# Kernel tuning notes

Measured on AMD Instinct MI355X. Metric: run time of the kernel, lower is better.

The kernel has to match this reference:

```python
import jax, jax.numpy as jnp
import numpy as np
from jax import lax

A = 15          # anchors per point
H = 34
W = 34
STRIDE = 8
ANCHOR_W = jnp.array([9.232984, 16.0, 27.712813, 18.465969, 32.0, 55.425626, 36.931937, 64.0, 110.851252, 73.863875, 128.0, 221.702503, 147.72775, 256.0, 443.405007], jnp.float32)
ANCHOR_H = jnp.array([27.72668, 16.0, 9.237604, 55.453359, 32.0, 18.475209, 110.906719, 64.0, 36.950417, 221.813438, 128.0, 73.900834, 443.626876, 256.0, 147.801669], jnp.float32)
BBOX_MEAN = jnp.array([0.000437, 0.002586, -0.123953, -0.081469], jnp.float32)
BBOX_STD = jnp.array([0.12677, 0.095741, 0.3173, 0.281042], jnp.float32)
THRESH = 0.2
MIN_H = 6.16056
MIN_W = 6.16056
MAX_CAND = 3000
TOP_N = 300
IOU_TH = 0.7
NEG = jnp.float32(-1e30)


def setup_inputs() -> dict:
    key = jax.random.key(0)
    k1, k2 = jax.random.split(key)
    return {
        "rpn_cls_prob_reshape": jax.random.uniform(k1, (1, 2 * A, H, W), jnp.float32),
        "rpn_bbox_pred": jax.random.normal(k2, (1, 4 * A, H, W), jnp.float32),
        "im_info": jnp.array([270, 270], jnp.int32),
    }


def reference(rpn_cls_prob_reshape, rpn_bbox_pred, im_info):
    origin_h = im_info[0].astype(jnp.float32)
    origin_w = im_info[1].astype(jnp.float32)
    # --- anchors: base boxes centered at origin, shifted over the grid ---
    xm = -0.5 * (ANCHOR_W - 1.0)
    ym = -0.5 * (ANCHOR_H - 1.0)
    base = jnp.stack([xm, ym, -xm, -ym], axis=1)  # [A,4] (xmin,ymin,xmax,ymax)
    sx = (jnp.arange(W) * STRIDE).astype(jnp.float32)
    sy = (jnp.arange(H) * STRIDE).astype(jnp.float32)
    SX, SY = jnp.meshgrid(sx, sy, indexing='ij')  # [W,H], matches torch meshgrid ij
    # original vstacks (shift_y, shift_x, shift_y, shift_x) -- replicate exactly
    shifts = jnp.stack([SY.ravel(), SX.ravel(), SY.ravel(), SX.ravel()], axis=1)  # [W*H,4]
    anchors = (shifts[:, None, :] + base[None, :, :]).reshape(-1, 4)  # [W*H*A,4]
    # --- bbox deltas: [1,4A,H,W] -> [(H*W*A),4] ---
    deltas = rpn_bbox_pred.reshape(A, 4, H, W).transpose(2, 3, 0, 1).reshape(-1, 4)
    deltas = deltas * BBOX_STD + BBOX_MEAN
    widths = anchors[:, 2] - anchors[:, 0] + 1.0
    heights = anchors[:, 3] - anchors[:, 1] + 1.0
    ctr_x = anchors[:, 0] + 0.5 * (widths - 1.0)
    ctr_y = anchors[:, 1] + 0.5 * (heights - 1.0)
    pcx = deltas[:, 0] * widths + ctr_x
    pcy = deltas[:, 1] * heights + ctr_y
    pw = jnp.exp(deltas[:, 2]) * widths
    ph = jnp.exp(deltas[:, 3]) * heights
    boxes = jnp.stack([pcx - 0.5 * (pw - 1.0), pcy - 0.5 * (ph - 1.0),
                       pcx + 0.5 * (pw - 1.0), pcy + 0.5 * (ph - 1.0)], axis=1)
    # --- clip to image (refine_out_of_map_bbox=True) ---
    boxes = jnp.stack([jnp.clip(boxes[:, 0], 0.0, origin_w - 1.0),
                       jnp.clip(boxes[:, 1], 0.0, origin_h - 1.0),
                       jnp.clip(boxes[:, 2], 0.0, origin_w - 1.0),
                       jnp.clip(boxes[:, 3], 0.0, origin_h - 1.0)], axis=1)
    # --- scores: [1,2A,H,W] -> [(H*W*A),2] ---
    scores = rpn_cls_prob_reshape.reshape(2, A, H * W).transpose(2, 1, 0).reshape(-1, 2)
    # --- filter: objectness threshold + HEIGHT_OR_WIDTH min size ---
    ws = boxes[:, 2] - boxes[:, 0] + 1.0
    hs = boxes[:, 3] - boxes[:, 1] + 1.0
    keep = (scores[:, 1] > THRESH) & ((ws >= MIN_W) | (hs >= MIN_H))
    masked = jnp.where(keep, scores[:, 1], NEG)
    top_vals, top_idx = lax.top_k(masked, MAX_CAND)
    cand_boxes = boxes[top_idx]       # [3000,4], sorted by desc score
    cand_scores = scores[top_idx]     # [3000,2]
    valid = top_vals > NEG * 0.5
    # --- greedy hard NMS (torchvision IoU convention, no +1) ---
    x1, y1, x2, y2 = cand_boxes[:, 0], cand_boxes[:, 1], cand_boxes[:, 2], cand_boxes[:, 3]
    areas = (x2 - x1) * (y2 - y1)
    iw = jnp.maximum(jnp.minimum(x2[:, None], x2[None, :]) - jnp.maximum(x1[:, None], x1[None, :]), 0.0)
    ih = jnp.maximum(jnp.minimum(y2[:, None], y2[None, :]) - jnp.maximum(y1[:, None], y1[None, :]), 0.0)
    inter = iw * ih
    iou = lax.stop_gradient(inter / jnp.maximum(areas[:, None] + areas[None, :] - inter, jnp.float32(1e-12)))
    pos = jnp.arange(MAX_CAND)

    def body(i, kp):
        sup = kp[i] & (iou[i] > IOU_TH) & (pos > i)
        return kp & ~sup

    kp = lax.fori_loop(0, MAX_CAND, body, valid)
    # --- take first top_n kept (score order preserved); pad with zeros ---
    sel = jnp.nonzero(kp, size=TOP_N, fill_value=MAX_CAND)[0]
    boxes_p = jnp.concatenate([cand_boxes, jnp.zeros((1, 4), cand_boxes.dtype)], axis=0)
    scores_p = jnp.concatenate([cand_scores, jnp.zeros((1, 2), cand_scores.dtype)], axis=0)
    out_boxes = boxes_p[sel]
    out_scores = scores_p[sel]
    proposals = jnp.concatenate([jnp.zeros((TOP_N, 1), out_boxes.dtype), out_boxes], axis=1)  # [300,5]
    return proposals, out_scores
```

## Files before the change

kernel.cpp:

```cpp
#include <hip/hip_runtime.h>
#include <stdint.h>

#define A 15
#define H_ 34
#define W_ 34
#define HW (H_*W_)
#define N (A*HW)
#define MAX_CAND 3000
#define TOP_N 300
#define NWORDS 47
#define CHUNK_W 3008
#define NBUCK 8000
#define JSLICE 8

__constant__ float c_aw[A] = {9.232984f, 16.0f, 27.712813f, 18.465969f, 32.0f, 55.425626f,
                              36.931937f, 64.0f, 110.851252f, 73.863875f, 128.0f, 221.702503f,
                              147.72775f, 256.0f, 443.405007f};
__constant__ float c_ah[A] = {27.72668f, 16.0f, 9.237604f, 55.453359f, 32.0f, 18.475209f,
                              110.906719f, 64.0f, 36.950417f, 221.813438f, 128.0f, 73.900834f,
                              443.626876f, 256.0f, 147.801669f};

__global__ __launch_bounds__(256) void k_boxes(
    const float* __restrict__ cls, const float* __restrict__ pred,
    const int* __restrict__ iminfo,
    float4* __restrict__ boxes, float2* __restrict__ scores,
    unsigned long long* __restrict__ keys)
{
    int m = blockIdx.x * 256 + threadIdx.x;
    if (m >= N) return;

    int a  = m % A;
    int hw = m / A;
    int w  = hw % W_;
    int h  = hw / W_;

    float ow = (float)iminfo[1];
    float oh = (float)iminfo[0];

    float aw = c_aw[a], ah = c_ah[a];
    float xm = __fmul_rn(-0.5f, __fsub_rn(aw, 1.0f));
    float ym = __fmul_rn(-0.5f, __fsub_rn(ah, 1.0f));
    float sxw = (float)(w * 8);
    float syh = (float)(h * 8);
    float x1 = __fadd_rn(sxw, xm);
    float y1 = __fadd_rn(syh, ym);
    float x2 = __fadd_rn(sxw, -xm);
    float y2 = __fadd_rn(syh, -ym);

    float widths  = __fadd_rn(__fsub_rn(x2, x1), 1.0f);
    float heights = __fadd_rn(__fsub_rn(y2, y1), 1.0f);
    float ctr_x = __fadd_rn(x1, __fmul_rn(0.5f, __fsub_rn(widths, 1.0f)));
    float ctr_y = __fadd_rn(y1, __fmul_rn(0.5f, __fsub_rn(heights, 1.0f)));

    const float std0 = 0.12677f,   std1 = 0.095741f, std2 = 0.3173f,    std3 = 0.281042f;
    const float mu0  = 0.000437f,  mu1  = 0.002586f, mu2  = -0.123953f, mu3  = -0.081469f;
    int pb = a * 4 * HW + hw;
    float d0 = __fadd_rn(__fmul_rn(pred[pb + 0 * HW], std0), mu0);
    float d1 = __fadd_rn(__fmul_rn(pred[pb + 1 * HW], std1), mu1);
    float d2 = __fadd_rn(__fmul_rn(pred[pb + 2 * HW], std2), mu2);
    float d3 = __fadd_rn(__fmul_rn(pred[pb + 3 * HW], std3), mu3);

    float pcx = __fadd_rn(__fmul_rn(d0, widths),  ctr_x);
    float pcy = __fadd_rn(__fmul_rn(d1, heights), ctr_y);
    float pw  = __fmul_rn(expf(d2), widths);
    float ph  = __fmul_rn(expf(d3), heights);

    float hpw = __fmul_rn(0.5f, __fsub_rn(pw, 1.0f));
    float hph = __fmul_rn(0.5f, __fsub_rn(ph, 1.0f));
    float bx1 = __fsub_rn(pcx, hpw);
    float by1 = __fsub_rn(pcy, hph);
    float bx2 = __fadd_rn(pcx, hpw);
    float by2 = __fadd_rn(pcy, hph);

    float ow1 = __fsub_rn(ow, 1.0f), oh1 = __fsub_rn(oh, 1.0f);
    bx1 = fminf(fmaxf(bx1, 0.0f), ow1);
    by1 = fminf(fmaxf(by1, 0.0f), oh1);
    bx2 = fminf(fmaxf(bx2, 0.0f), ow1);
    by2 = fminf(fmaxf(by2, 0.0f), oh1);

    float s0 = cls[a * HW + hw];
    float s1 = cls[(A + a) * HW + hw];

    float wsv = __fadd_rn(__fsub_rn(bx2, bx1), 1.0f);
    float hsv = __fadd_rn(__fsub_rn(by2, by1), 1.0f);
    bool keep = (s1 > 0.2f) && ((wsv >= 6.16056f) || (hsv >= 6.16056f));
    float masked = keep ? s1 : -1e30f;

    boxes[m]  = make_float4(bx1, by1, bx2, by2);
    scores[m] = make_float2(s0, s1);

    int bucket = keep ? (1 + min(NBUCK - 2, max(0, (int)(s1 * (float)(NBUCK - 2))))) : 0;
    unsigned int fb = __float_as_uint(masked);
    fb = (fb & 0x80000000u) ? ~fb : (fb | 0x80000000u);
    keys[m] = ((unsigned long long)bucket << 51)
            | ((unsigned long long)fb << 15)
            | (unsigned long long)((~m) & 0x7fff);
}

__global__ __launch_bounds__(1024) void k_mid(
    const unsigned long long* __restrict__ keys,
    const float4* __restrict__ boxes, const float2* __restrict__ scores,
    unsigned long long* __restrict__ skeys,
    float4* __restrict__ cboxes, float2* __restrict__ cscores,
    unsigned long long* __restrict__ kpm)
{
    __shared__ int s_base[NBUCK];
    __shared__ int s_off[NBUCK];
    __shared__ unsigned long long s_kpm[NWORDS];
    __shared__ int s_B[1];

    const int t = threadIdx.x;

    for (int k = t; k < NBUCK; k += 1024) s_base[k] = 0;
    if (t < NWORDS) s_kpm[t] = 0ull;
    __syncthreads();

    unsigned long long myk[17];
    #pragma unroll
    for (int q = 0; q < 17; ++q) {
        int i = q * 1024 + t;
        myk[q] = (i < N) ? keys[i] : 0ull;
        if (i < N) atomicAdd(&s_base[(int)(myk[q] >> 51)], 1);
    }
    __syncthreads();

    int c0=0,c1=0,c2=0,c3=0,c4=0,c5=0,c6=0,c7=0;
    int gsum = 0;
    const int g0 = t * 8;
    if (t < NBUCK / 8) {
        c0 = s_base[g0+0]; c1 = s_base[g0+1]; c2 = s_base[g0+2]; c3 = s_base[g0+3];
        c4 = s_base[g0+4]; c5 = s_base[g0+5]; c6 = s_base[g0+6]; c7 = s_base[g0+7];
        gsum = c0+c1+c2+c3+c4+c5+c6+c7;
    }
    int* tsum = s_off;
    tsum[t] = gsum;
    __syncthreads();
    for (int d = 1; d < 1024; d <<= 1) {
        int v = (t + d < 1024) ? tsum[t + d] : 0;
        __syncthreads();
        tsum[t] += v;
        __syncthreads();
    }
    int above = (t < 1023) ? tsum[t + 1] : 0;

    if (t < NBUCK / 8) {
        int run = above;
        #define STEP(q, cq) { s_base[g0+q] = run; \
            if (run < MAX_CAND && run + cq >= MAX_CAND) s_B[0] = g0 + q; \
            run += cq; }
        STEP(7, c7) STEP(6, c6) STEP(5, c5) STEP(4, c4)
        STEP(3, c3) STEP(2, c2) STEP(1, c1) STEP(0, c0)
        #undef STEP
    }
    __syncthreads();
    const int B = s_B[0];
    for (int k = t; k < NBUCK; k += 1024) s_off[k] = 0;
    __syncthreads();

    #pragma unroll
    for (int q = 0; q < 17; ++q) {
        int i = q * 1024 + t;
        if (i < N) {
            int b = (int)(myk[q] >> 51);
            if (b >= B) {
                int slot = s_base[b] + atomicAdd(&s_off[b], 1);
                skeys[slot] = myk[q];
            }
        }
    }
    __syncthreads();
    const int S = s_base[B] + s_off[B];

    for (int p = t; p < S; p += 1024) {
        unsigned long long k = skeys[p];
        int b  = (int)(k >> 51);
        int lo = s_base[b];
        int hi = lo + s_off[b];
        int cg = 0;
        for (int j = lo; j < hi; ++j) cg += (skeys[j] > k) ? 1 : 0;
        int rank = lo + cg;
        if (rank < MAX_CAND) {
            int orig = ((int)k & 0x7fff) ^ 0x7fff;
            cboxes[rank]  = boxes[orig];
            cscores[rank] = scores[orig];
            if (b >= 1) atomicOr(&s_kpm[rank >> 6], 1ull << (rank & 63));
        }
    }
    __syncthreads();
    if (t < NWORDS) kpm[t] = s_kpm[t];
}

__device__ __forceinline__ bool iou_gt(
    float4 bi, float ai, float4 bj, float aj)
{
    float iw = fmaxf(__fsub_rn(fminf(bi.z, bj.z), fmaxf(bi.x, bj.x)), 0.0f);
    float ih = fmaxf(__fsub_rn(fminf(bi.w, bj.w), fmaxf(bi.y, bj.y)), 0.0f);
    float inter = __fmul_rn(iw, ih);
    float denom = fmaxf(__fsub_rn(__fadd_rn(ai, aj), inter), 1e-12f);
    return (inter / denom) > 0.7f;
}

__global__ __launch_bounds__(1024) void k_iou(
    const float4* __restrict__ cboxes, unsigned long long* __restrict__ sup)
{
    __shared__ float4 bx[MAX_CAND];
    int t = threadIdx.x;
    for (int k = t; k < MAX_CAND; k += 1024) bx[k] = cboxes[k];
    __syncthreads();

    const int lane = t & 63;
    const int wave = t >> 6;
    const int c = blockIdx.x;
    const int s = blockIdx.y;
    const int r0 = c * 64 + wave * 4;

    float4 bi[4]; float ai[4];
    #pragma unroll
    for (int u = 0; u < 4; ++u) {
        int rc = min(r0 + u, MAX_CAND - 1);
        bi[u] = bx[rc];
        ai[u] = __fmul_rn(__fsub_rn(bi[u].z, bi[u].x), __fsub_rn(bi[u].w, bi[u].y));
    }

    for (int w = c + s; w < NWORDS; w += JSLICE) {
        int jc = w * 64 + lane;
        bool jv = (jc < MAX_CAND);
        float4 bj = bx[jv ? jc : (MAX_CAND - 1)];
        float  aj = __fmul_rn(__fsub_rn(bj.z, bj.x), __fsub_rn(bj.w, bj.y));
        #pragma unroll
        for (int u = 0; u < 4; ++u) {
            int r = r0 + u;
            bool p = jv && (r < MAX_CAND) && (jc > r) && iou_gt(bi[u], ai[u], bj, aj);
            unsigned long long msk = __ballot(p);
            if (lane == 0 && r < MAX_CAND) sup[(size_t)r * NWORDS + w] = msk;
        }
    }
}

__global__ __launch_bounds__(1024) void k_nms_out(
    const unsigned long long* __restrict__ sup,
    const unsigned long long* __restrict__ kpm,
    const float4* __restrict__ cboxes, const float2* __restrict__ cscores,
    float* __restrict__ out)
{
    __shared__ unsigned long long buf[2][CHUNK_W];
    __shared__ unsigned long long kp[NWORDS + 1];
    __shared__ int sel[TOP_N];
    __shared__ int s_stop;

    int tid  = threadIdx.x;
    int lane = tid & 63;
    int wave = tid >> 6;

    for (int t = tid; t < TOP_N * 7; t += 1024) out[t] = 0.0f;
    for (int t = tid; t < TOP_N; t += 1024) sel[t] = -1;

    if (tid < NWORDS) kp[tid] = kpm[tid];

    {
        unsigned long long v0 = sup[tid];
        unsigned long long v1 = sup[tid + 1024];
        unsigned long long v2 = (tid + 2048 < CHUNK_W) ? sup[tid + 2048] : 0ull;
        buf[0][tid] = v0;
        buf[0][tid + 1024] = v1;
        if (tid + 2048 < CHUNK_W) buf[0][tid + 2048] = v2;
    }
    __syncthreads();

    int kept_total = 0;
    for (int w = 0; w < NWORDS; ++w) {
        int cur = w & 1;
        bool havnext = (w + 1 < NWORDS);

        unsigned long long v0 = 0, v1 = 0, v2 = 0;
        if (havnext) {
            const unsigned long long* src = sup + (size_t)(w + 1) * CHUNK_W;
            v0 = src[tid];
            v1 = src[tid + 1024];
            v2 = (tid + 2048 < CHUNK_W) ? src[tid + 2048] : 0ull;
        }

        if (wave == 0) {
            unsigned long long intra = buf[cur][lane * NWORDS + w];
            unsigned long long nz = __ballot(intra != 0ull);
            unsigned long long kw = kp[w];
            unsigned long long rem = kw & nz;
            while (rem) {
                int b = __ffsll((long long)rem) - 1;
                rem &= rem - 1;
                if ((kw >> b) & 1ull) {
                    unsigned long long row = __shfl(intra, b, 64);
                    kw  &= ~row;
                    rem &= ~row;
                }
            }
            if (lane == 0) kp[w] = kw;
            kept_total += __popcll(kw);
            bool stop = (kept_total >= TOP_N) || !havnext;
            if (lane == 0) s_stop = stop ? 1 : 0;

            if (!stop && lane < NWORDS && lane > w) {
                unsigned long long comb = 0;
                #pragma unroll 8
                for (int b = 0; b < 64; ++b) {
                    unsigned long long r = buf[cur][b * NWORDS + lane];
                    if ((kw >> b) & 1ull) comb |= r;
                }
                kp[lane] &= ~comb;
            }
        }

        if (havnext) {
            int nxt = cur ^ 1;
            buf[nxt][tid] = v0;
            buf[nxt][tid + 1024] = v1;
            if (tid + 2048 < CHUNK_W) buf[nxt][tid + 2048] = v2;
        }
        __syncthreads();
        if (s_stop) break;
    }

    if (wave == 0) {
        unsigned long long kw = (lane < NWORDS) ? kp[lane] : 0ull;
        int cnt = __popcll(kw);
        int pre = cnt;
        for (int d = 1; d < 64; d <<= 1) {
            int o = __shfl_up(pre, d, 64);
            if (lane >= d) pre += o;
        }
        int prefix = pre - cnt;
        while (kw && prefix < TOP_N) {
            int b = __ffsll((long long)kw) - 1;
            kw &= kw - 1;
            sel[prefix] = lane * 64 + b;
            prefix++;
        }
    }
    __syncthreads();

    if (tid < TOP_N) {
        int j = sel[tid];
        if (j >= 0) {
            float4 bx = cboxes[j];
            float2 sc = cscores[j];
            out[tid * 5 + 0] = 0.0f;
            out[tid * 5 + 1] = bx.x;
            out[tid * 5 + 2] = bx.y;
            out[tid * 5 + 3] = bx.z;
            out[tid * 5 + 4] = bx.w;
            out[TOP_N * 5 + tid * 2 + 0] = sc.x;
            out[TOP_N * 5 + tid * 2 + 1] = sc.y;
        }
    }
}

extern "C" void kernel_launch(void* const* d_in, const int* in_sizes, int n_in,
                              void* d_out, int out_size, void* d_ws, size_t ws_size,
                              hipStream_t stream) {
    const float* cls    = (const float*)d_in[0];
    const float* pred   = (const float*)d_in[1];
    const int*   iminfo = (const int*)d_in[2];
    float* out = (float*)d_out;

    char* p = (char*)d_ws;
    auto alloc = [&](size_t bytes) -> char* {
        char* q = p;
        p += (bytes + 255) & ~(size_t)255;
        return q;
    };
    float4* boxes  = (float4*)alloc((size_t)N * sizeof(float4));
    float2* scores = (float2*)alloc((size_t)N * sizeof(float2));
    unsigned long long* keys  = (unsigned long long*)alloc((size_t)N * 8);
    unsigned long long* skeys = (unsigned long long*)alloc((size_t)N * 8);
    float4* cboxes  = (float4*)alloc((size_t)MAX_CAND * sizeof(float4));
    float2* cscores = (float2*)alloc((size_t)MAX_CAND * sizeof(float2));
    unsigned long long* kpm = (unsigned long long*)alloc((size_t)NWORDS * 8);
    unsigned long long* sup = (unsigned long long*)alloc((size_t)MAX_CAND * NWORDS * 8);

    int nb = (N + 255) / 256;
    k_boxes <<<nb, 256, 0, stream>>>(cls, pred, iminfo, boxes, scores, keys);
    k_mid   <<<1, 1024, 0, stream>>>(keys, boxes, scores, skeys, cboxes, cscores, kpm);
    k_iou   <<<dim3(NWORDS, JSLICE), 1024, 0, stream>>>(cboxes, sup);
    k_nms_out<<<1, 1024, 0, stream>>>(sup, kpm, cboxes, cscores, out);
}
```

Before: 114.9 us.

## Use wave-shuffle scan, keep sorted keys in LDS, drop LDS staging in IoU

The block-wide suffix scan in k_mid, which used many __syncthreads barriers, is replaced by a wave shuffle scan plus a small cross-wave total. The bucketed candidate keys are kept in shared memory up to a capacity of 4224, so the rank-counting loop reads LDS instead of global memory, with a global fallback for overflow. k_iou no longer copies all 3000 boxes into LDS per block and reads them straight from global/cache instead. The extra LDS in k_mid may reduce occupancy, though it runs as a single block.

```diff
diff --git a/kernel.cpp b/kernel.cpp
--- a/kernel.cpp
+++ b/kernel.cpp
@@ -12,6 +12,7 @@
 #define CHUNK_W 3008
 #define NBUCK 8000
 #define JSLICE 8
+#define SCAP 4224
 
 __constant__ float c_aw[A] = {9.232984f, 16.0f, 27.712813f, 18.465969f, 32.0f, 55.425626f,
                               36.931937f, 64.0f, 110.851252f, 73.863875f, 128.0f, 221.702503f,
@@ -106,12 +107,16 @@
 {
     __shared__ int s_base[NBUCK];
     __shared__ int s_off[NBUCK];
+    __shared__ unsigned long long s_keys[SCAP];
     __shared__ unsigned long long s_kpm[NWORDS];
+    __shared__ int s_wtot[16];
     __shared__ int s_B[1];
 
-    const int t = threadIdx.x;
-
-    for (int k = t; k < NBUCK; k += 1024) s_base[k] = 0;
+    const int t    = threadIdx.x;
+    const int lane = t & 63;
+    const int wv   = t >> 6;
+
+    for (int k = t; k < NBUCK; k += 1024) { s_base[k] = 0; s_off[k] = 0; }
     if (t < NWORDS) s_kpm[t] = 0ull;
     __syncthreads();
 
@@ -132,16 +137,19 @@
         c4 = s_base[g0+4]; c5 = s_base[g0+5]; c6 = s_base[g0+6]; c7 = s_base[g0+7];
         gsum = c0+c1+c2+c3+c4+c5+c6+c7;
     }
-    int* tsum = s_off;
-    tsum[t] = gsum;
-    __syncthreads();
-    for (int d = 1; d < 1024; d <<= 1) {
-        int v = (t + d < 1024) ? tsum[t + d] : 0;
-        __syncthreads();
-        tsum[t] += v;
-        __syncthreads();
-    }
-    int above = (t < 1023) ? tsum[t + 1] : 0;
+    int sfx = gsum;
+    #pragma unroll
+    for (int d = 1; d < 64; d <<= 1) {
+        int v = __shfl_down(sfx, d, 64);
+        if (lane + d < 64) sfx += v;
+    }
+    int wtot = __shfl(sfx, 0, 64);
+    if (lane == 0) s_wtot[wv] = wtot;
+    __syncthreads();
+    int later = 0;
+    #pragma unroll
+    for (int u = 0; u < 16; ++u) if (u > wv) later += s_wtot[u];
+    int above = (sfx + later) - gsum;
 
     if (t < NBUCK / 8) {
         int run = above;
@@ -154,8 +162,6 @@
     }
     __syncthreads();
     const int B = s_B[0];
-    for (int k = t; k < NBUCK; k += 1024) s_off[k] = 0;
-    __syncthreads();
 
     #pragma unroll
     for (int q = 0; q < 17; ++q) {
@@ -164,7 +170,8 @@
             int b = (int)(myk[q] >> 51);
             if (b >= B) {
                 int slot = s_base[b] + atomicAdd(&s_off[b], 1);
-                skeys[slot] = myk[q];
+                if (slot < SCAP) s_keys[slot] = myk[q];
+                else             skeys[slot]  = myk[q];
             }
         }
     }
@@ -172,12 +179,15 @@
     const int S = s_base[B] + s_off[B];
 
     for (int p = t; p < S; p += 1024) {
-        unsigned long long k = skeys[p];
+        unsigned long long k = (p < SCAP) ? s_keys[p] : skeys[p];
         int b  = (int)(k >> 51);
         int lo = s_base[b];
         int hi = lo + s_off[b];
         int cg = 0;
-        for (int j = lo; j < hi; ++j) cg += (skeys[j] > k) ? 1 : 0;
+        for (int j = lo; j < hi; ++j) {
+            unsigned long long kj = (j < SCAP) ? s_keys[j] : skeys[j];
+            cg += (kj > k) ? 1 : 0;
+        }
         int rank = lo + cg;
         if (rank < MAX_CAND) {
             int orig = ((int)k & 0x7fff) ^ 0x7fff;
@@ -203,11 +213,7 @@
 __global__ __launch_bounds__(1024) void k_iou(
     const float4* __restrict__ cboxes, unsigned long long* __restrict__ sup)
 {
-    __shared__ float4 bx[MAX_CAND];
-    int t = threadIdx.x;
-    for (int k = t; k < MAX_CAND; k += 1024) bx[k] = cboxes[k];
-    __syncthreads();
-
+    const int t    = threadIdx.x;
     const int lane = t & 63;
     const int wave = t >> 6;
     const int c = blockIdx.x;
@@ -218,14 +224,14 @@
     #pragma unroll
     for (int u = 0; u < 4; ++u) {
         int rc = min(r0 + u, MAX_CAND - 1);
-        bi[u] = bx[rc];
+        bi[u] = cboxes[rc];
         ai[u] = __fmul_rn(__fsub_rn(bi[u].z, bi[u].x), __fsub_rn(bi[u].w, bi[u].y));
     }
 
     for (int w = c + s; w < NWORDS; w += JSLICE) {
         int jc = w * 64 + lane;
         bool jv = (jc < MAX_CAND);
-        float4 bj = bx[jv ? jc : (MAX_CAND - 1)];
+        float4 bj = cboxes[jv ? jc : (MAX_CAND - 1)];
         float  aj = __fmul_rn(__fsub_rn(bj.z, bj.x), __fsub_rn(bj.w, bj.y));
         #pragma unroll
         for (int u = 0; u < 4; ++u) {
```

Result: faster. 111.6 us (-2.9%).
